# Kernel optimization log

Hardware: AMD Instinct MI355X
Metric: run time of the kernel (lower is better)

## Reference

```python
import jax, jax.numpy as jnp
import numpy as np

N_NODES = 50000
N_EDGES = 800000
D_IN, D_H1, D_H2 = 256, 128, 64


def setup_inputs() -> dict:
    key = jax.random.key(0)
    k1, k2, k3, k4, k5, k6, k7 = jax.random.split(key, 7)
    x = jax.random.normal(k1, (N_NODES, D_IN), dtype=jnp.float32)
    edge_index = jax.random.randint(k2, (2, N_EDGES), 0, N_NODES, dtype=jnp.int64)
    edge_weight = jax.random.uniform(k3, (N_EDGES,), dtype=jnp.float32)
    # GCNConv params: Linear (no bias) weight + separate bias, Glorot-ish scale
    W1 = jax.random.normal(k4, (D_IN, D_H1), dtype=jnp.float32) / np.sqrt(D_IN)
    b1 = jnp.zeros((D_H1,), dtype=jnp.float32)
    W2 = jax.random.normal(k5, (D_H1, D_H2), dtype=jnp.float32) / np.sqrt(D_H1)
    b2 = jnp.zeros((D_H2,), dtype=jnp.float32)
    return {"x": x, "edge_index": edge_index, "edge_weight": edge_weight,
            "W1": W1, "b1": b1, "W2": W2, "b2": b2}


def _gcn_norm(edge_index, edge_weight, n_nodes):
    # PyG gcn_norm: add self-loops (weight 1), symmetric D^-1/2 A D^-1/2
    loops = jnp.arange(n_nodes, dtype=edge_index.dtype)
    src = jnp.concatenate([edge_index[0], loops])
    dst = jnp.concatenate([edge_index[1], loops])
    w = jnp.concatenate([edge_weight, jnp.ones((n_nodes,), edge_weight.dtype)])
    deg = jax.ops.segment_sum(w, dst, num_segments=n_nodes)
    dinv = jnp.where(deg > 0, jax.lax.rsqrt(deg), 0.0)
    norm = dinv[src] * w * dinv[dst]  # [E+N]
    return src, dst, norm


def _gcn_conv(h, src, dst, norm, W, b, n_nodes):
    h = h @ W                                   # [N, d_out] dense GEMM
    msg = h[src] * norm[:, None]                # gather + scale  [E+N, d_out]
    out = jax.ops.segment_sum(msg, dst, num_segments=n_nodes)  # scatter-add
    return out + b


def reference(x, edge_index, edge_weight, W1, b1, W2, b2):
    n = x.shape[0]
    src, dst, norm = _gcn_norm(edge_index, edge_weight, n)
    # dropout p=0 -> identity
    h = jax.nn.relu(_gcn_conv(x, src, dst, norm, W1, b1, n))
    h = jax.nn.relu(_gcn_conv(h, src, dst, norm, W2, b2, n))
    return h
```

## Files before the change

kernel.cpp:

```cpp
#include <hip/hip_runtime.h>


static constexpr int SCAN_CHUNK = 1024;
static constexpr int CPAD = 16;

using short8 = __attribute__((ext_vector_type(8))) short;
using f32x4  = __attribute__((ext_vector_type(4))) float;

__device__ inline unsigned short bf16rne(float f) {
  unsigned u = __float_as_uint(f);
  u += 0x7fffu + ((u >> 16) & 1u);
  return (unsigned short)(u >> 16);
}
__device__ inline float bflo(unsigned u) { return __uint_as_float(u << 16); }
__device__ inline float bfhi(unsigned u) { return __uint_as_float(u & 0xffff0000u); }

__device__ inline void wtp_pack(const float* __restrict__ W,
                                unsigned short* __restrict__ Wtp,
                                int i, int K, int C) {
  int e = i & 7;
  int l = (i >> 3) & 63;
  int rest = i >> 9;
  int NT = C / 16;
  int nt = rest % NT;
  int kc = rest / NT;
  int k = kc * 32 + (l >> 4) * 8 + e;
  int n = nt * 16 + (l & 15);
  Wtp[i] = bf16rne(W[(size_t)k * C + n]);
}

__global__ __launch_bounds__(256) void k_prep(int* __restrict__ cnt, int nz,
                                              const float* __restrict__ W1,
                                              unsigned short* __restrict__ wtp1,
                                              const float* __restrict__ W2,
                                              unsigned short* __restrict__ wtp2) {
  int i = blockIdx.x * 256 + threadIdx.x;
  if (i < nz) cnt[i] = 0;
  if (i < 256 * 128) wtp_pack(W1, wtp1, i, 256, 128);
  if (i < 128 * 64) wtp_pack(W2, wtp2, i, 128, 64);
}

__global__ __launch_bounds__(256, 3) void k_count_gemm1(
    const int* __restrict__ dst, int* __restrict__ cnt, int* __restrict__ epos,
    int E, int CB,
    const float* __restrict__ A, const unsigned short* __restrict__ Wtp,
    unsigned short* __restrict__ H, int n) {
  if (blockIdx.x < CB) {
    const int base = blockIdx.x * 1024 + threadIdx.x;
    int d[4];
#pragma unroll
    for (int j = 0; j < 4; ++j) {
      int e = base + j * 256;
      d[j] = (e < E) ? dst[e] : -1;
    }
#pragma unroll
    for (int j = 0; j < 4; ++j) {
      int e = base + j * 256;
      if (e < E) epos[e] = atomicAdd(&cnt[(size_t)d[j] * CPAD], 1);
    }
    return;
  }
  constexpr int K = 256, C = 128, NT = C / 16, KCH = K / 32;
  const int w = threadIdx.x >> 6;
  const int l = threadIdx.x & 63;
  const int lm = l & 15;
  const int lk = (l >> 4) * 8;
  const int row0 = ((blockIdx.x - CB) * 4 + w) * 16;
  if (row0 >= n) return;
  const int m = row0 + lm;
  const bool valid = m < n;
  const size_t arow = (size_t)(valid ? m : 0) * K;

  short8 af[KCH];
  {
    float4 a[2 * KCH];
#pragma unroll
    for (int c = 0; c < KCH; ++c) {
      if (valid) {
        a[2 * c]     = *(const float4*)(A + arow + c * 32 + lk);
        a[2 * c + 1] = *(const float4*)(A + arow + c * 32 + lk + 4);
      } else {
        a[2 * c] = a[2 * c + 1] = make_float4(0.f, 0.f, 0.f, 0.f);
      }
    }
#pragma unroll
    for (int c = 0; c < KCH; ++c) {
      af[c][0] = (short)bf16rne(a[2 * c].x);     af[c][1] = (short)bf16rne(a[2 * c].y);
      af[c][2] = (short)bf16rne(a[2 * c].z);     af[c][3] = (short)bf16rne(a[2 * c].w);
      af[c][4] = (short)bf16rne(a[2 * c + 1].x); af[c][5] = (short)bf16rne(a[2 * c + 1].y);
      af[c][6] = (short)bf16rne(a[2 * c + 1].z); af[c][7] = (short)bf16rne(a[2 * c + 1].w);
    }
  }
  f32x4 acc[NT] = {};
  const short8* B = (const short8*)Wtp;
#pragma unroll
  for (int c = 0; c < KCH; ++c)
#pragma unroll
    for (int nt = 0; nt < NT; ++nt)
      acc[nt] = __builtin_amdgcn_mfma_f32_16x16x32_bf16(af[c], B[(c * NT + nt) * 64 + l],
                                                        acc[nt], 0, 0, 0);
  const int orow = row0 + (l >> 4) * 4;
#pragma unroll
  for (int nt = 0; nt < NT; ++nt)
#pragma unroll
    for (int r = 0; r < 4; ++r) {
      int g = orow + r;
      if (g < n) H[(size_t)g * C + nt * 16 + lm] = bf16rne(acc[nt][r]);
    }
}

__global__ __launch_bounds__(256) void k_scan1(const int* __restrict__ in,
                                               int* __restrict__ out,
                                               int* __restrict__ sums, int n) {
  __shared__ int sd[256];
  const int base = blockIdx.x * SCAN_CHUNK;
  const int tid = threadIdx.x;
  int v[4], tot = 0;
#pragma unroll
  for (int j = 0; j < 4; ++j) {
    int idx = base + tid * 4 + j;
    v[j] = (idx < n) ? in[(size_t)idx * CPAD] : 0;
    tot += v[j];
  }
  sd[tid] = tot;
  __syncthreads();
  for (int d = 1; d < 256; d <<= 1) {
    int t = (tid >= d) ? sd[tid - d] : 0;
    __syncthreads();
    sd[tid] += t;
    __syncthreads();
  }
  if (tid == 255) sums[blockIdx.x] = sd[255];
  int run = sd[tid] - tot;
#pragma unroll
  for (int j = 0; j < 4; ++j) {
    int idx = base + tid * 4 + j;
    if (idx < n) out[idx] = run;
    run += v[j];
  }
}

__global__ __launch_bounds__(64) void k_scan2(int* __restrict__ sums, int n) {
  int tid = threadIdx.x;
  int o = (tid < n) ? sums[tid] : 0;
  int v = o;
  for (int d = 1; d < 64; d <<= 1) {
    int t = __shfl_up(v, d, 64);
    if (tid >= d) v += t;
  }
  if (tid < n) sums[tid] = v - o;
}

__global__ __launch_bounds__(256) void k_bucket2(const int* __restrict__ src,
                                                 const int* __restrict__ dst,
                                                 const float* __restrict__ w,
                                                 const int* __restrict__ row_ptr,
                                                 const int* __restrict__ chunks,
                                                 const int* __restrict__ epos,
                                                 int2* __restrict__ csr, int E) {
  int e = blockIdx.x * 256 + threadIdx.x;
  if (e < E) {
    int d = dst[e];
    int pos = row_ptr[d] + chunks[d >> 10] + epos[e];
    csr[pos] = make_int2(src[e], __float_as_int(w[e]));
  }
}

__global__ __launch_bounds__(256) void k_deg_dinv(const int* __restrict__ row_ptr,
                                                  const int* __restrict__ chunks,
                                                  const int2* __restrict__ csr,
                                                  float* __restrict__ dinv, int n) {
  int i = blockIdx.x * 256 + threadIdx.x;
  if (i >= n) return;
  const int e0 = row_ptr[i] + chunks[i >> 10];
  const int e1 = row_ptr[i + 1] + chunks[(i + 1) >> 10];
  float s = 1.0f;
  int e = e0;
  for (; e + 4 <= e1; e += 4) {
    float w0 = __int_as_float(csr[e].y), w1 = __int_as_float(csr[e + 1].y);
    float w2 = __int_as_float(csr[e + 2].y), w3 = __int_as_float(csr[e + 3].y);
    s += (w0 + w1) + (w2 + w3);
  }
  for (; e < e1; ++e) s += __int_as_float(csr[e].y);
  dinv[i] = rsqrtf(s);
}

__global__ __launch_bounds__(256) void k_finalize(int2* __restrict__ csr,
                                                  const float* __restrict__ dinv,
                                                  int E) {
  int e = blockIdx.x * 256 + threadIdx.x;
  if (e < E) {
    int2 c = csr[e];
    c.y = __float_as_int(__int_as_float(c.y) * dinv[c.x]);
    csr[e] = c;
  }
}

template <int K, int C>
__global__ __launch_bounds__(256, 4) void k_gemm_bf(
    const unsigned short* __restrict__ A, const unsigned short* __restrict__ Wtp,
    unsigned short* __restrict__ H, int n) {
  constexpr int NT = C / 16, KCH = K / 32;
  const int w = threadIdx.x >> 6;
  const int l = threadIdx.x & 63;
  const int lm = l & 15;
  const int lk = (l >> 4) * 8;
  const int row0 = (blockIdx.x * 4 + w) * 16;
  if (row0 >= n) return;
  const int m = row0 + lm;
  const bool valid = m < n;
  const size_t arow = (size_t)(valid ? m : 0) * K;
  short8 af[KCH];
#pragma unroll
  for (int c = 0; c < KCH; ++c)
    af[c] = valid ? *(const short8*)(A + arow + c * 32 + lk)
                  : short8{0, 0, 0, 0, 0, 0, 0, 0};
  f32x4 acc[NT] = {};
  const short8* B = (const short8*)Wtp;
#pragma unroll
  for (int c = 0; c < KCH; ++c)
#pragma unroll
    for (int nt = 0; nt < NT; ++nt)
      acc[nt] = __builtin_amdgcn_mfma_f32_16x16x32_bf16(af[c], B[(c * NT + nt) * 64 + l],
                                                        acc[nt], 0, 0, 0);
  const int orow = row0 + (l >> 4) * 4;
#pragma unroll
  for (int nt = 0; nt < NT; ++nt)
#pragma unroll
    for (int r = 0; r < 4; ++r) {
      int g = orow + r;
      if (g < n) H[(size_t)g * C + nt * 16 + lm] = bf16rne(acc[nt][r]);
    }
}

template <int C, bool OUTF32>
__global__ __launch_bounds__(256) void k_aggregate(
    const int* __restrict__ row_ptr, const int* __restrict__ chunks,
    const int2* __restrict__ csr, const unsigned short* __restrict__ h,
    const float* __restrict__ dinv, const float* __restrict__ bias,
    void* __restrict__ outp, int n) {
  constexpr int LPN = C / 8;
  constexpr int NPB = 256 / LPN;
  const int g = threadIdx.x % LPN;
  const int i = blockIdx.x * NPB + threadIdx.x / LPN;
  if (i >= n) return;
  const float di = dinv[i];
  const uint4* h4 = (const uint4*)h;
  uint4 hv = h4[(size_t)i * LPN + g];
  float a0 = di * bflo(hv.x), a1 = di * bfhi(hv.x);
  float a2 = di * bflo(hv.y), a3 = di * bfhi(hv.y);
  float a4 = di * bflo(hv.z), a5 = di * bfhi(hv.z);
  float a6 = di * bflo(hv.w), a7 = di * bfhi(hv.w);
  const int e1 = row_ptr[i + 1] + chunks[(i + 1) >> 10];
  int e = row_ptr[i] + chunks[i >> 10];
  for (; e + 8 <= e1; e += 8) {
    int2 c[8];
    uint4 v[8];
#pragma unroll
    for (int j = 0; j < 8; ++j) c[j] = csr[e + j];
#pragma unroll
    for (int j = 0; j < 8; ++j) v[j] = h4[(size_t)c[j].x * LPN + g];
#pragma unroll
    for (int j = 0; j < 8; ++j) {
      float wj = __int_as_float(c[j].y);
      a0 = fmaf(bflo(v[j].x), wj, a0); a1 = fmaf(bfhi(v[j].x), wj, a1);
      a2 = fmaf(bflo(v[j].y), wj, a2); a3 = fmaf(bfhi(v[j].y), wj, a3);
      a4 = fmaf(bflo(v[j].z), wj, a4); a5 = fmaf(bfhi(v[j].z), wj, a5);
      a6 = fmaf(bflo(v[j].w), wj, a6); a7 = fmaf(bfhi(v[j].w), wj, a7);
    }
  }
  for (; e + 4 <= e1; e += 4) {
    int2 c[4];
    uint4 v[4];
#pragma unroll
    for (int j = 0; j < 4; ++j) c[j] = csr[e + j];
#pragma unroll
    for (int j = 0; j < 4; ++j) v[j] = h4[(size_t)c[j].x * LPN + g];
#pragma unroll
    for (int j = 0; j < 4; ++j) {
      float wj = __int_as_float(c[j].y);
      a0 = fmaf(bflo(v[j].x), wj, a0); a1 = fmaf(bfhi(v[j].x), wj, a1);
      a2 = fmaf(bflo(v[j].y), wj, a2); a3 = fmaf(bfhi(v[j].y), wj, a3);
      a4 = fmaf(bflo(v[j].z), wj, a4); a5 = fmaf(bfhi(v[j].z), wj, a5);
      a6 = fmaf(bflo(v[j].w), wj, a6); a7 = fmaf(bfhi(v[j].w), wj, a7);
    }
  }
  for (; e < e1; ++e) {
    int2 c = csr[e];
    float wj = __int_as_float(c.y);
    uint4 v = h4[(size_t)c.x * LPN + g];
    a0 = fmaf(bflo(v.x), wj, a0); a1 = fmaf(bfhi(v.x), wj, a1);
    a2 = fmaf(bflo(v.y), wj, a2); a3 = fmaf(bfhi(v.y), wj, a3);
    a4 = fmaf(bflo(v.z), wj, a4); a5 = fmaf(bfhi(v.z), wj, a5);
    a6 = fmaf(bflo(v.w), wj, a6); a7 = fmaf(bfhi(v.w), wj, a7);
  }
  const float4* b4 = (const float4*)bias;
  float4 bb0 = b4[g * 2], bb1 = b4[g * 2 + 1];
  a0 = fmaxf(fmaf(a0, di, bb0.x), 0.f); a1 = fmaxf(fmaf(a1, di, bb0.y), 0.f);
  a2 = fmaxf(fmaf(a2, di, bb0.z), 0.f); a3 = fmaxf(fmaf(a3, di, bb0.w), 0.f);
  a4 = fmaxf(fmaf(a4, di, bb1.x), 0.f); a5 = fmaxf(fmaf(a5, di, bb1.y), 0.f);
  a6 = fmaxf(fmaf(a6, di, bb1.z), 0.f); a7 = fmaxf(fmaf(a7, di, bb1.w), 0.f);
  if (OUTF32) {
    float4* o4 = (float4*)outp;
    o4[(size_t)i * (C / 4) + g * 2]     = make_float4(a0, a1, a2, a3);
    o4[(size_t)i * (C / 4) + g * 2 + 1] = make_float4(a4, a5, a6, a7);
  } else {
    uint4 o;
    o.x = (unsigned)bf16rne(a0) | ((unsigned)bf16rne(a1) << 16);
    o.y = (unsigned)bf16rne(a2) | ((unsigned)bf16rne(a3) << 16);
    o.z = (unsigned)bf16rne(a4) | ((unsigned)bf16rne(a5) << 16);
    o.w = (unsigned)bf16rne(a6) | ((unsigned)bf16rne(a7) << 16);
    ((uint4*)outp)[(size_t)i * LPN + g] = o;
  }
}

extern "C" void kernel_launch(void* const* d_in, const int* in_sizes, int n_in,
                              void* d_out, int out_size, void* d_ws, size_t ws_size,
                              hipStream_t stream) {
  (void)n_in; (void)out_size; (void)ws_size;
  const float* x  = (const float*)d_in[0];
  const int*   ei = (const int*)d_in[1];
  const float* ew = (const float*)d_in[2];
  const float* W1 = (const float*)d_in[3];
  const float* b1 = (const float*)d_in[4];
  const float* W2 = (const float*)d_in[5];
  const float* b2 = (const float*)d_in[6];
  float* out = (float*)d_out;

  const int N = in_sizes[0] / 256;
  const int E = in_sizes[2];
  const int* src = ei;
  const int* dst = ei + E;

  float* ws      = (float*)d_ws;
  float* dinv    = ws;
  int*   row_ptr = (int*)(ws + 50176);
  int*   chunks  = row_ptr + 50176;
  int*   cnt     = chunks + 256;
  int*   epos    = cnt + 800256;
  int2*  csr     = (int2*)(epos + 800256);
  unsigned short* h1   = (unsigned short*)((int*)csr + 2 * 800256);
  unsigned short* o1   = h1 + (size_t)50000 * 128;
  unsigned short* wtp1 = o1 + (size_t)50000 * 128;
  unsigned short* wtp2 = wtp1 + 128 * 256;
  unsigned short* h2   = h1;

  const int nz = (N + 1) * CPAD;
  const int nchunks = (N + 1 + SCAN_CHUNK - 1) / SCAN_CHUNK;
  const int CB = (E + 1023) / 1024;
  const int GB = (N + 63) / 64;

  k_prep<<<(nz + 255) / 256, 256, 0, stream>>>(cnt, nz, W1, wtp1, W2, wtp2);
  k_count_gemm1<<<CB + GB, 256, 0, stream>>>(dst, cnt, epos, E, CB, x, wtp1, h1, N);
  k_scan1<<<nchunks, 256, 0, stream>>>(cnt, row_ptr, chunks, N + 1);
  k_scan2<<<1, 64, 0, stream>>>(chunks, nchunks);
  k_bucket2<<<(E + 255) / 256, 256, 0, stream>>>(src, dst, ew, row_ptr, chunks,
                                                 epos, csr, E);
  k_deg_dinv<<<(N + 255) / 256, 256, 0, stream>>>(row_ptr, chunks, csr, dinv, N);
  k_finalize<<<(E + 255) / 256, 256, 0, stream>>>(csr, dinv, E);

  k_aggregate<128, false><<<(N + 15) / 16, 256, 0, stream>>>(row_ptr, chunks, csr,
                                                             h1, dinv, b1, o1, N);
  k_gemm_bf<128, 64><<<(N + 63) / 64, 256, 0, stream>>>(o1, wtp2, h2, N);
  k_aggregate<64, true><<<(N + 31) / 32, 256, 0, stream>>>(row_ptr, chunks, csr,
                                                           h2, dinv, b2, out, N);
}
```

Before: 151.3 us.

## Fold dinv edge scaling into aggregation and interleave count/GEMM blocks

```diff
diff --git a/kernel.cpp b/kernel.cpp
--- a/kernel.cpp
+++ b/kernel.cpp
@@ -40,13 +40,15 @@
   if (i < 128 * 64) wtp_pack(W2, wtp2, i, 128, 64);
 }
 
-__global__ __launch_bounds__(256, 3) void k_count_gemm1(
+__global__ __launch_bounds__(256, 4) void k_count_gemm1(
     const int* __restrict__ dst, int* __restrict__ cnt, int* __restrict__ epos,
     int E, int CB,
     const float* __restrict__ A, const unsigned short* __restrict__ Wtp,
     unsigned short* __restrict__ H, int n) {
-  if (blockIdx.x < CB) {
-    const int base = blockIdx.x * 1024 + threadIdx.x;
+  const int bid = blockIdx.x;
+  const int wid = bid >> 1;
+  if ((bid & 1) == 0) {
+    const int base = wid * 1024 + threadIdx.x;
     int d[4];
 #pragma unroll
     for (int j = 0; j < 4; ++j) {
@@ -65,7 +67,7 @@
   const int l = threadIdx.x & 63;
   const int lm = l & 15;
   const int lk = (l >> 4) * 8;
-  const int row0 = ((blockIdx.x - CB) * 4 + w) * 16;
+  const int row0 = (wid * 4 + w) * 16;
   if (row0 >= n) return;
   const int m = row0 + lm;
   const bool valid = m < n;
@@ -183,17 +185,6 @@
   }
   for (; e < e1; ++e) s += __int_as_float(csr[e].y);
   dinv[i] = rsqrtf(s);
-}
-
-__global__ __launch_bounds__(256) void k_finalize(int2* __restrict__ csr,
-                                                  const float* __restrict__ dinv,
-                                                  int E) {
-  int e = blockIdx.x * 256 + threadIdx.x;
-  if (e < E) {
-    int2 c = csr[e];
-    c.y = __float_as_int(__int_as_float(c.y) * dinv[c.x]);
-    csr[e] = c;
-  }
 }
 
 template <int K, int C>
@@ -256,13 +247,16 @@
   for (; e + 8 <= e1; e += 8) {
     int2 c[8];
     uint4 v[8];
+    float ds[8];
 #pragma unroll
     for (int j = 0; j < 8; ++j) c[j] = csr[e + j];
 #pragma unroll
     for (int j = 0; j < 8; ++j) v[j] = h4[(size_t)c[j].x * LPN + g];
 #pragma unroll
+    for (int j = 0; j < 8; ++j) ds[j] = dinv[c[j].x];
+#pragma unroll
     for (int j = 0; j < 8; ++j) {
-      float wj = __int_as_float(c[j].y);
+      float wj = __int_as_float(c[j].y) * ds[j];
       a0 = fmaf(bflo(v[j].x), wj, a0); a1 = fmaf(bfhi(v[j].x), wj, a1);
       a2 = fmaf(bflo(v[j].y), wj, a2); a3 = fmaf(bfhi(v[j].y), wj, a3);
       a4 = fmaf(bflo(v[j].z), wj, a4); a5 = fmaf(bfhi(v[j].z), wj, a5);
@@ -272,13 +266,16 @@
   for (; e + 4 <= e1; e += 4) {
     int2 c[4];
     uint4 v[4];
+    float ds[4];
 #pragma unroll
     for (int j = 0; j < 4; ++j) c[j] = csr[e + j];
 #pragma unroll
     for (int j = 0; j < 4; ++j) v[j] = h4[(size_t)c[j].x * LPN + g];
 #pragma unroll
+    for (int j = 0; j < 4; ++j) ds[j] = dinv[c[j].x];
+#pragma unroll
     for (int j = 0; j < 4; ++j) {
-      float wj = __int_as_float(c[j].y);
+      float wj = __int_as_float(c[j].y) * ds[j];
       a0 = fmaf(bflo(v[j].x), wj, a0); a1 = fmaf(bfhi(v[j].x), wj, a1);
       a2 = fmaf(bflo(v[j].y), wj, a2); a3 = fmaf(bfhi(v[j].y), wj, a3);
       a4 = fmaf(bflo(v[j].z), wj, a4); a5 = fmaf(bfhi(v[j].z), wj, a5);
@@ -287,7 +284,7 @@
   }
   for (; e < e1; ++e) {
     int2 c = csr[e];
-    float wj = __int_as_float(c.y);
+    float wj = __int_as_float(c.y) * dinv[c.x];
     uint4 v = h4[(size_t)c.x * LPN + g];
     a0 = fmaf(bflo(v.x), wj, a0); a1 = fmaf(bfhi(v.x), wj, a1);
     a2 = fmaf(bflo(v.y), wj, a2); a3 = fmaf(bfhi(v.y), wj, a3);
@@ -357,7 +354,6 @@
   k_bucket2<<<(E + 255) / 256, 256, 0, stream>>>(src, dst, ew, row_ptr, chunks,
                                                  epos, csr, E);
   k_deg_dinv<<<(N + 255) / 256, 256, 0, stream>>>(row_ptr, chunks, csr, dinv, N);
-  k_finalize<<<(E + 255) / 256, 256, 0, stream>>>(csr, dinv, E);
 
   k_aggregate<128, false><<<(N + 15) / 16, 256, 0, stream>>>(row_ptr, chunks, csr,
                                                              h1, dinv, b1, o1, N);
```

After: 136.7 us, median of 2. 1.11x faster.
